# Optimization experiments

Hardware: AMD Instinct MI355X
Metric: run time of the kernel (lower is better)

Reference implementation:

```python
import jax, jax.numpy as jnp
import numpy as np


def setup_inputs() -> dict:
    key = jax.random.key(0)
    ks = jax.random.split(key, 8)
    B, C, D, H, W = 4, 128, 16, 16, 16
    Cqk = C // 8  # out_channels // 8 = 16
    return {
        "x": jax.random.normal(ks[0], (B, C, D, H, W), dtype=jnp.float32),
        "Wq": jax.random.normal(ks[1], (Cqk, C), dtype=jnp.float32) * 0.05,
        "bq": jax.random.normal(ks[2], (Cqk,), dtype=jnp.float32) * 0.05,
        "Wk": jax.random.normal(ks[3], (Cqk, C), dtype=jnp.float32) * 0.05,
        "bk": jax.random.normal(ks[4], (Cqk,), dtype=jnp.float32) * 0.05,
        "Wv": jax.random.normal(ks[5], (C, C), dtype=jnp.float32) * 0.05,
        "bv": jax.random.normal(ks[6], (C,), dtype=jnp.float32) * 0.05,
        "gamma": jax.random.normal(ks[7], (1,), dtype=jnp.float32),
    }


def reference(x, Wq, bq, Wk, bk, Wv, bv, gamma):
    B, C, D, H, W = x.shape
    xf = x.reshape(B, C, D * H * W)  # b c n
    # 1x1x1 Conv3d == channel-wise GEMM
    q = jnp.einsum('oc,bcn->bon', Wq, xf) + bq[None, :, None]  # [B, Cqk, N]
    k = jnp.einsum('oc,bcn->bon', Wk, xf) + bk[None, :, None]  # [B, Cqk, N]
    v = jnp.einsum('oc,bcn->bon', Wv, xf) + bv[None, :, None]  # [B, C,   N]
    # attention[b, n, m] = sum_c q[b,c,n] * k[b,c,m]  (NO 1/sqrt(d) scaling, faithful)
    attn = jax.nn.softmax(jnp.einsum('bcn,bcm->bnm', q, k), axis=-1)  # [B, N, N]
    out = jnp.einsum('bcm,bnm->bcn', v, attn)  # [B, C, N]
    out = out.reshape(B, C, D, H, W)
    return gamma * out + x
```

## Files before the change

### kernel.cpp

```cpp
#include <hip/hip_runtime.h>


typedef __attribute__((ext_vector_type(8))) short short8;
typedef __attribute__((ext_vector_type(4))) float f32x4;

#define NTOK 4096
#define CDIM 128
#define L2E 1.44269504088896340736f

__device__ __forceinline__ unsigned short f2bf(float f) {
  unsigned int u = __float_as_uint(f);
  return (unsigned short)((u + 0x7fffu + ((u >> 16) & 1u)) >> 16);
}

__global__ __launch_bounds__(256) void sa3d_proj(
    const float* __restrict__ x,
    const float* __restrict__ Wq, const float* __restrict__ bq,
    const float* __restrict__ Wk, const float* __restrict__ bk,
    const float* __restrict__ Wv, const float* __restrict__ bv,
    unsigned short* __restrict__ qb, unsigned short* __restrict__ kb,
    unsigned short* __restrict__ vb)
{
  __shared__ unsigned short Wl[160 * 136];
  __shared__ unsigned short xT[64 * 136];
  const int tid = threadIdx.x;
  const int b = (blockIdx.x & 7) >> 1;
  const int nt = ((blockIdx.x >> 3) << 1) | (blockIdx.x & 1);
  const int n0 = nt << 6;

  for (int i = 0; i < 80; ++i) {
    int idx = i * 256 + tid;
    int o = idx >> 7, c = idx & 127;
    float wv;
    if (o < 16)      wv = Wq[o * 128 + c] * L2E;
    else if (o < 32) wv = Wk[(o - 16) * 128 + c];
    else             wv = Wv[(o - 32) * 128 + c];
    Wl[o * 136 + c] = f2bf(wv);
  }
  {
    int nn = tid & 63, cg = tid >> 6;
    const float* xp = x + (size_t)b * CDIM * NTOK + n0 + nn;
    for (int cp = 0; cp < 16; ++cp) {
      int c = cg * 32 + cp * 2;
      float v0 = xp[(size_t)c * NTOK];
      float v1 = xp[(size_t)(c + 1) * NTOK];
      *(unsigned int*)&xT[nn * 136 + c] =
          (unsigned int)f2bf(v0) | ((unsigned int)f2bf(v1) << 16);
    }
  }
  __syncthreads();

  const int w = tid >> 6, lane = tid & 63;
  const int l15 = lane & 15, g = lane >> 4;

  short8 bfr[4];
#pragma unroll
  for (int ks = 0; ks < 4; ++ks)
    bfr[ks] = *(const short8*)&xT[(w * 16 + l15) * 136 + ks * 32 + g * 8];

  const int n = n0 + w * 16 + l15;
#pragma unroll
  for (int ot = 0; ot < 10; ++ot) {
    f32x4 acc = {};
#pragma unroll
    for (int ks = 0; ks < 4; ++ks) {
      short8 af = *(const short8*)&Wl[(ot * 16 + l15) * 136 + ks * 32 + g * 8];
      acc = __builtin_amdgcn_mfma_f32_16x16x32_bf16(af, bfr[ks], acc, 0, 0, 0);
    }
    int ob = ot * 16 + 4 * g;
    if (ot == 0) {
      unsigned int p0 = (unsigned int)f2bf(acc[0] + bq[ob] * L2E) |
                        ((unsigned int)f2bf(acc[1] + bq[ob + 1] * L2E) << 16);
      unsigned int p1 = (unsigned int)f2bf(acc[2] + bq[ob + 2] * L2E) |
                        ((unsigned int)f2bf(acc[3] + bq[ob + 3] * L2E) << 16);
      unsigned int* d = (unsigned int*)&qb[((size_t)b * NTOK + n) * 16 + ob];
      d[0] = p0; d[1] = p1;
    } else if (ot == 1) {
      int o2 = ob - 16;
      unsigned int p0 = (unsigned int)f2bf(acc[0] + bk[o2]) |
                        ((unsigned int)f2bf(acc[1] + bk[o2 + 1]) << 16);
      unsigned int p1 = (unsigned int)f2bf(acc[2] + bk[o2 + 2]) |
                        ((unsigned int)f2bf(acc[3] + bk[o2 + 3]) << 16);
      unsigned int* d = (unsigned int*)&kb[((size_t)b * NTOK + n) * 16 + o2];
      d[0] = p0; d[1] = p1;
    } else {
#pragma unroll
      for (int r = 0; r < 4; ++r) {
        int o = ob + r - 32;
        size_t eidx = (size_t)(n >> 6) * 8192 +
                      (size_t)((o >> 4) * 2 + ((n >> 5) & 1)) * 512 +
                      (size_t)((n >> 3) & 3) * 128 + (o & 15) * 8 + (n & 7);
        vb[(size_t)b * (CDIM * NTOK) + eidx] = f2bf(acc[r] + bv[o]);
      }
    }
  }
}

__global__ __launch_bounds__(512, 2) void sa3d_attn(
    const unsigned short* __restrict__ qb, const unsigned short* __restrict__ kb,
    const unsigned short* __restrict__ vb,
    const float* __restrict__ x, const float* __restrict__ gamma,
    float* __restrict__ out)
{
  __shared__ __align__(16) unsigned char smem[37888];

  const int tid = threadIdx.x;
  const int w = tid >> 6, lane = tid & 63;
  const int l15 = lane & 15, g = lane >> 4;
  const int kg = w >> 1, cg = w & 1;
  const int b = (blockIdx.x & 7) >> 1;
  const int qt = ((blockIdx.x >> 3) << 1) | (blockIdx.x & 1);
  const int q0 = qt << 5;

  unsigned short* PLk = (unsigned short*)smem + kg * 4608;
  float* LDp = (float*)(smem + 36864);

  const unsigned short* qbase = qb + (size_t)b * NTOK * 16;
  const unsigned short* kbase = kb + (size_t)b * NTOK * 16;
  const unsigned short* vbase = vb + (size_t)b * CDIM * NTOK;

  short8 aq[2] = {short8{}, short8{}};
#pragma unroll
  for (int qh = 0; qh < 2; ++qh)
    if (g < 2)
      aq[qh] = *(const short8*)&qbase[(size_t)(q0 + qh * 16 + l15) * 16 + g * 8];

  f32x4 acc[8];
#pragma unroll
  for (int i = 0; i < 8; ++i) acc[i] = (f32x4){};
  float Lp[2][4] = {{0.f, 0.f, 0.f, 0.f}, {0.f, 0.f, 0.f, 0.f}};

  const int kv0 = kg << 10;
  const int kcolb = cg * 32 + l15;
  const int voff = cg * 4096 + g * 128 + l15 * 8;
  const unsigned short* vtile = vbase + (size_t)kg * 16 * 8192;

  short8 kf[2];

#define LOADK(TT)                                                             \
  {                                                                           \
    _Pragma("unroll") for (int j = 0; j < 2; ++j) {                           \
      kf[j] = short8{};                                                       \
      if (g < 2)                                                              \
        kf[j] = *(const short8*)&kbase[                                       \
            (size_t)(kv0 + ((TT) << 6) + kcolb + j * 16) * 16 + g * 8];       \
    }                                                                         \
  }

#define SA_PRODUCE(TN)                                                        \
  {                                                                           \
    const int pbn = ((TN) & 1) * 2304;                                        \
    _Pragma("unroll") for (int j = 0; j < 2; ++j) {                           \
      _Pragma("unroll") for (int qh = 0; qh < 2; ++qh) {                      \
        f32x4 z = {};                                                         \
        f32x4 s = __builtin_amdgcn_mfma_f32_16x16x32_bf16(aq[qh], kf[j],      \
                                                          z, 0, 0, 0);        \
        float e0 = __builtin_exp2f(s[0]);                                     \
        float e1 = __builtin_exp2f(s[1]);                                     \
        float e2 = __builtin_exp2f(s[2]);                                     \
        float e3 = __builtin_exp2f(s[3]);                                     \
        Lp[qh][0] += e0; Lp[qh][1] += e1;                                     \
        Lp[qh][2] += e2; Lp[qh][3] += e3;                                     \
        unsigned int pk0, pk1;                                                \
        asm("v_cvt_pk_bf16_f32 %0, %1, %2" : "=v"(pk0) : "v"(e0), "v"(e1));   \
        asm("v_cvt_pk_bf16_f32 %0, %1, %2" : "=v"(pk1) : "v"(e2), "v"(e3));   \
        const int rb = pbn + (qh * 16 + 4 * g) * 72 + kcolb + j * 16;         \
        PLk[rb]       = (unsigned short)pk0;                                  \
        PLk[rb + 72]  = (unsigned short)(pk0 >> 16);                          \
        PLk[rb + 144] = (unsigned short)pk1;                                  \
        PLk[rb + 216] = (unsigned short)(pk1 >> 16);                          \
      }                                                                       \
    }                                                                         \
  }

#define SA_ITER(T, PROD, PREF)                                                \
  {                                                                           \
    const int pbo = ((T) & 1) * 2304;                                         \
    short8 pa0[2];                                                            \
    _Pragma("unroll") for (int ch = 0; ch < 2; ++ch)                          \
      pa0[ch] = *(const short8*)&PLk[pbo + l15 * 72 + ch * 32 + g * 8];       \
    short8 vf[8];                                                             \
    {                                                                         \
      const unsigned short* vt = vtile + (size_t)(T) * 8192;                  \
      _Pragma("unroll") for (int f = 0; f < 8; ++f)                           \
        vf[f] = *(const short8*)&vt[f * 512 + voff];                          \
    }                                                                         \
    if (PROD) SA_PRODUCE((T) + 1);                                            \
    if (PREF) LOADK((T) + 2);                                                 \
    __builtin_amdgcn_s_setprio(1);                                            \
    _Pragma("unroll") for (int ctl = 0; ctl < 4; ++ctl)                       \
      _Pragma("unroll") for (int ch = 0; ch < 2; ++ch)                        \
        acc[ctl] = __builtin_amdgcn_mfma_f32_16x16x32_bf16(                   \
            pa0[ch], vf[ctl * 2 + ch], acc[ctl], 0, 0, 0);                    \
    __builtin_amdgcn_s_setprio(0);                                            \
    short8 pa1[2];                                                            \
    _Pragma("unroll") for (int ch = 0; ch < 2; ++ch)                          \
      pa1[ch] = *(const short8*)&PLk[pbo + (16 + l15) * 72 + ch * 32 + g * 8];\
    __builtin_amdgcn_s_setprio(1);                                            \
    _Pragma("unroll") for (int ctl = 0; ctl < 4; ++ctl)                       \
      _Pragma("unroll") for (int ch = 0; ch < 2; ++ch)                        \
        acc[4 + ctl] = __builtin_amdgcn_mfma_f32_16x16x32_bf16(               \
            pa1[ch], vf[ctl * 2 + ch], acc[4 + ctl], 0, 0, 0);                \
    __builtin_amdgcn_s_setprio(0);                                            \
    __syncthreads();                                                          \
  }

  LOADK(0);
  SA_PRODUCE(0);
  LOADK(1);
  __syncthreads();

  for (int tt = 0; tt < 7; ++tt) {
    SA_ITER(2 * tt, 1, 1);
    SA_ITER(2 * tt + 1, 1, 1);
  }
  SA_ITER(14, 1, 0);
  SA_ITER(15, 0, 0);
#undef SA_PRODUCE
#undef SA_ITER
#undef LOADK

#pragma unroll
  for (int qh = 0; qh < 2; ++qh)
#pragma unroll
    for (int r = 0; r < 4; ++r) {
      float v = Lp[qh][r];
      v += __shfl_xor(v, 1);
      v += __shfl_xor(v, 2);
      v += __shfl_xor(v, 4);
      v += __shfl_xor(v, 8);
      Lp[qh][r] = v;
    }
  if (l15 == 0) {
#pragma unroll
    for (int qh = 0; qh < 2; ++qh)
#pragma unroll
      for (int r = 0; r < 4; ++r)
        LDp[w * 32 + qh * 16 + 4 * g + r] = Lp[qh][r];
  }
  __syncthreads();

  const int rowb = lane * 128;
  const int sw = (l15 & 7) << 4;

#define ACC_STORE(i)                                                        \
  {                                                                         \
    char* base = (char*)smem + (i) * 8192 + rowb;                           \
    _Pragma("unroll") for (int j = 0; j < 8; ++j)                           \
        *(f32x4*)(base + ((j * 16) ^ sw)) = acc[j];                         \
  }
#define ACC_ADD(i)                                                          \
  {                                                                         \
    char* base = (char*)smem + (i) * 8192 + rowb;                           \
    _Pragma("unroll") for (int j = 0; j < 8; ++j)                           \
        acc[j] += *(const f32x4*)(base + ((j * 16) ^ sw));                  \
  }

  if (w >= 4) ACC_STORE(w - 4);
  __syncthreads();
  if (w < 4) ACC_ADD(w);
  __syncthreads();
  if (w == 2 || w == 3) ACC_STORE(w - 2);
  __syncthreads();

  if (w < 2) {
    ACC_ADD(w);
    float Lf[2][4] = {{0.f, 0.f, 0.f, 0.f}, {0.f, 0.f, 0.f, 0.f}};
#pragma unroll
    for (int w8 = 0; w8 < 8; ++w8)
#pragma unroll
      for (int qh = 0; qh < 2; ++qh)
#pragma unroll
        for (int r = 0; r < 4; ++r)
          Lf[qh][r] += LDp[w8 * 32 + qh * 16 + 4 * g + r];
    const float ga = gamma[0];
    float inv[2][4];
#pragma unroll
    for (int qh = 0; qh < 2; ++qh)
#pragma unroll
      for (int r = 0; r < 4; ++r) inv[qh][r] = 1.0f / Lf[qh][r];

    const float* xb = x + (size_t)b * CDIM * NTOK;
    float* ob = out + (size_t)b * CDIM * NTOK;
#pragma unroll
    for (int qh = 0; qh < 2; ++qh)
#pragma unroll
      for (int ctl = 0; ctl < 4; ++ctl) {
        int c = w * 64 + ctl * 16 + l15;
        size_t idx = (size_t)c * NTOK + q0 + qh * 16 + 4 * g;
        f32x4 xv = *(const f32x4*)&xb[idx];
        f32x4 o;
#pragma unroll
        for (int r = 0; r < 4; ++r)
          o[r] = ga * acc[qh * 4 + ctl][r] * inv[qh][r] + xv[r];
        *(f32x4*)&ob[idx] = o;
      }
  }
}

extern "C" void kernel_launch(void* const* d_in, const int* in_sizes, int n_in,
                              void* d_out, int out_size, void* d_ws, size_t ws_size,
                              hipStream_t stream) {
  const float* x     = (const float*)d_in[0];
  const float* Wq    = (const float*)d_in[1];
  const float* bq    = (const float*)d_in[2];
  const float* Wk    = (const float*)d_in[3];
  const float* bk    = (const float*)d_in[4];
  const float* Wv    = (const float*)d_in[5];
  const float* bv    = (const float*)d_in[6];
  const float* gamma = (const float*)d_in[7];

  unsigned short* qb = (unsigned short*)d_ws;
  unsigned short* kb = qb + (size_t)4 * NTOK * 16;
  unsigned short* vb = kb + (size_t)4 * NTOK * 16;
  float* outp = (float*)d_out;

  sa3d_proj<<<dim3(256), dim3(256), 0, stream>>>(x, Wq, bq, Wk, bk, Wv, bv,
                                                 qb, kb, vb);
  sa3d_attn<<<dim3(512), dim3(512), 0, stream>>>(qb, kb, vb, x, gamma, outp);
}
```

Before: 69.67 us.

## Keep softmax probabilities in registers via transposed QK MFMA and lane shuffles

Computes S^T with K as the MFMA A operand so each wave produces the full probability tile for its own key range. It then rearranges the packed bf16 values into the PV A-operand layout with cross-lane shuffles instead of staging them through LDS. This removes the LDS P buffers and the per-tile __syncthreads, and shrinks shared memory. In exchange each wave now computes the QK^T tile for all 64 keys of a tile (double the QK MFMAs and exps per wave) and adds shuffle traffic and serial dependency between QK and PV within a wave.

```diff
diff --git a/kernel.cpp b/kernel.cpp
--- a/kernel.cpp
+++ b/kernel.cpp
@@ -3,6 +3,7 @@
 
 typedef __attribute__((ext_vector_type(8))) short short8;
 typedef __attribute__((ext_vector_type(4))) float f32x4;
+typedef __attribute__((ext_vector_type(4))) unsigned int u32x4;
 
 #define NTOK 4096
 #define CDIM 128
@@ -102,7 +103,7 @@
     const float* __restrict__ x, const float* __restrict__ gamma,
     float* __restrict__ out)
 {
-  __shared__ __align__(16) unsigned char smem[37888];
+  __shared__ __align__(16) unsigned char smem[33792];
 
   const int tid = threadIdx.x;
   const int w = tid >> 6, lane = tid & 63;
@@ -112,8 +113,7 @@
   const int qt = ((blockIdx.x >> 3) << 1) | (blockIdx.x & 1);
   const int q0 = qt << 5;
 
-  unsigned short* PLk = (unsigned short*)smem + kg * 4608;
-  float* LDp = (float*)(smem + 36864);
+  float* LDp = (float*)(smem + 32768);
 
   const unsigned short* qbase = qb + (size_t)b * NTOK * 16;
   const unsigned short* kbase = kb + (size_t)b * NTOK * 16;
@@ -128,109 +128,103 @@
   f32x4 acc[8];
 #pragma unroll
   for (int i = 0; i < 8; ++i) acc[i] = (f32x4){};
-  float Lp[2][4] = {{0.f, 0.f, 0.f, 0.f}, {0.f, 0.f, 0.f, 0.f}};
+  float Lq[2] = {0.f, 0.f};
 
   const int kv0 = kg << 10;
-  const int kcolb = cg * 32 + l15;
   const int voff = cg * 4096 + g * 128 + l15 * 8;
   const unsigned short* vtile = vbase + (size_t)kg * 16 * 8192;
 
-  short8 kf[2];
+  const bool hi32 = lane >= 32;
+  const int srcb = l15 + ((g & 1) << 5);
+
+  short8 kf[4];
 
 #define LOADK(TT)                                                             \
   {                                                                           \
-    _Pragma("unroll") for (int j = 0; j < 2; ++j) {                           \
+    _Pragma("unroll") for (int j = 0; j < 4; ++j) {                           \
       kf[j] = short8{};                                                       \
       if (g < 2)                                                              \
         kf[j] = *(const short8*)&kbase[                                       \
-            (size_t)(kv0 + ((TT) << 6) + kcolb + j * 16) * 16 + g * 8];       \
+            (size_t)(kv0 + ((TT) << 6) + j * 16 + l15) * 16 + g * 8];         \
     }                                                                         \
   }
 
-#define SA_PRODUCE(TN)                                                        \
+#define QK_HALF(HC, PA)                                                       \
   {                                                                           \
-    const int pbn = ((TN) & 1) * 2304;                                        \
-    _Pragma("unroll") for (int j = 0; j < 2; ++j) {                           \
+    unsigned int cpk[2][2][2];                           \
+    _Pragma("unroll") for (int kt2 = 0; kt2 < 2; ++kt2) {                     \
       _Pragma("unroll") for (int qh = 0; qh < 2; ++qh) {                      \
         f32x4 z = {};                                                         \
-        f32x4 s = __builtin_amdgcn_mfma_f32_16x16x32_bf16(aq[qh], kf[j],      \
-                                                          z, 0, 0, 0);        \
+        f32x4 s = __builtin_amdgcn_mfma_f32_16x16x32_bf16(                    \
+            kf[(HC) * 2 + kt2], aq[qh], z, 0, 0, 0);                          \
         float e0 = __builtin_exp2f(s[0]);                                     \
         float e1 = __builtin_exp2f(s[1]);                                     \
         float e2 = __builtin_exp2f(s[2]);                                     \
         float e3 = __builtin_exp2f(s[3]);                                     \
-        Lp[qh][0] += e0; Lp[qh][1] += e1;                                     \
-        Lp[qh][2] += e2; Lp[qh][3] += e3;                                     \
-        unsigned int pk0, pk1;                                                \
-        asm("v_cvt_pk_bf16_f32 %0, %1, %2" : "=v"(pk0) : "v"(e0), "v"(e1));   \
-        asm("v_cvt_pk_bf16_f32 %0, %1, %2" : "=v"(pk1) : "v"(e2), "v"(e3));   \
-        const int rb = pbn + (qh * 16 + 4 * g) * 72 + kcolb + j * 16;         \
-        PLk[rb]       = (unsigned short)pk0;                                  \
-        PLk[rb + 72]  = (unsigned short)(pk0 >> 16);                          \
-        PLk[rb + 144] = (unsigned short)pk1;                                  \
-        PLk[rb + 216] = (unsigned short)(pk1 >> 16);                          \
+        Lq[qh] += (e0 + e1) + (e2 + e3);                                      \
+        asm("v_cvt_pk_bf16_f32 %0, %1, %2"                                    \
+            : "=v"(cpk[qh][kt2][0]) : "v"(e0), "v"(e1));                      \
+        asm("v_cvt_pk_bf16_f32 %0, %1, %2"                                    \
+            : "=v"(cpk[qh][kt2][1]) : "v"(e2), "v"(e3));                      \
       }                                                                       \
     }                                                                         \
-  }
-
-#define SA_ITER(T, PROD, PREF)                                                \
+    _Pragma("unroll") for (int qh = 0; qh < 2; ++qh) {                        \
+      unsigned int selA = hi32 ? cpk[qh][1][0] : cpk[qh][0][0];               \
+      unsigned int selB = hi32 ? cpk[qh][1][1] : cpk[qh][0][1];               \
+      unsigned int w0 = (unsigned int)__shfl((int)selA, srcb);                \
+      unsigned int w1 = (unsigned int)__shfl((int)selB, srcb);                \
+      unsigned int w2 = (unsigned int)__shfl((int)selA, srcb + 16);           \
+      unsigned int w3 = (unsigned int)__shfl((int)selB, srcb + 16);           \
+      u32x4 pw = {w0, w1, w2, w3};                                            \
+      PA[qh] = *(short8*)&pw;                                                 \
+    }                                                                         \
+  }
+
+#define SA_TILE(T, PREF)                                                      \
   {                                                                           \
-    const int pbo = ((T) & 1) * 2304;                                         \
-    short8 pa0[2];                                                            \
-    _Pragma("unroll") for (int ch = 0; ch < 2; ++ch)                          \
-      pa0[ch] = *(const short8*)&PLk[pbo + l15 * 72 + ch * 32 + g * 8];       \
     short8 vf[8];                                                             \
     {                                                                         \
       const unsigned short* vt = vtile + (size_t)(T) * 8192;                  \
       _Pragma("unroll") for (int f = 0; f < 8; ++f)                           \
         vf[f] = *(const short8*)&vt[f * 512 + voff];                          \
     }                                                                         \
-    if (PROD) SA_PRODUCE((T) + 1);                                            \
-    if (PREF) LOADK((T) + 2);                                                 \
+    short8 pa[2];                                                             \
+    QK_HALF(0, pa);                                                           \
     __builtin_amdgcn_s_setprio(1);                                            \
-    _Pragma("unroll") for (int ctl = 0; ctl < 4; ++ctl)                       \
-      _Pragma("unroll") for (int ch = 0; ch < 2; ++ch)                        \
-        acc[ctl] = __builtin_amdgcn_mfma_f32_16x16x32_bf16(                   \
-            pa0[ch], vf[ctl * 2 + ch], acc[ctl], 0, 0, 0);                    \
+    _Pragma("unroll") for (int qh = 0; qh < 2; ++qh)                          \
+      _Pragma("unroll") for (int ctl = 0; ctl < 4; ++ctl)                     \
+        acc[qh * 4 + ctl] = __builtin_amdgcn_mfma_f32_16x16x32_bf16(          \
+            pa[qh], vf[ctl * 2 + 0], acc[qh * 4 + ctl], 0, 0, 0);             \
     __builtin_amdgcn_s_setprio(0);                                            \
-    short8 pa1[2];                                                            \
-    _Pragma("unroll") for (int ch = 0; ch < 2; ++ch)                          \
-      pa1[ch] = *(const short8*)&PLk[pbo + (16 + l15) * 72 + ch * 32 + g * 8];\
+    QK_HALF(1, pa);                                                           \
+    if (PREF) LOADK((T) + 1);                                                 \
     __builtin_amdgcn_s_setprio(1);                                            \
-    _Pragma("unroll") for (int ctl = 0; ctl < 4; ++ctl)                       \
-      _Pragma("unroll") for (int ch = 0; ch < 2; ++ch)                        \
-        acc[4 + ctl] = __builtin_amdgcn_mfma_f32_16x16x32_bf16(               \
-            pa1[ch], vf[ctl * 2 + ch], acc[4 + ctl], 0, 0, 0);                \
+    _Pragma("unroll") for (int qh = 0; qh < 2; ++qh)                          \
+      _Pragma("unroll") for (int ctl = 0; ctl < 4; ++ctl)                     \
+        acc[qh * 4 + ctl] = __builtin_amdgcn_mfma_f32_16x16x32_bf16(          \
+            pa[qh], vf[ctl * 2 + 1], acc[qh * 4 + ctl], 0, 0, 0);             \
     __builtin_amdgcn_s_setprio(0);                                            \
-    __syncthreads();                                                          \
   }
 
   LOADK(0);
-  SA_PRODUCE(0);
-  LOADK(1);
-  __syncthreads();
-
-  for (int tt = 0; tt < 7; ++tt) {
-    SA_ITER(2 * tt, 1, 1);
-    SA_ITER(2 * tt + 1, 1, 1);
-  }
-  SA_ITER(14, 1, 0);
-  SA_ITER(15, 0, 0);
-#undef SA_PRODUCE
-#undef SA_ITER
+  SA_TILE(0, 1);  SA_TILE(1, 1);  SA_TILE(2, 1);  SA_TILE(3, 1);
+  SA_TILE(4, 1);  SA_TILE(5, 1);  SA_TILE(6, 1);  SA_TILE(7, 1);
+  SA_TILE(8, 1);  SA_TILE(9, 1);  SA_TILE(10, 1); SA_TILE(11, 1);
+  SA_TILE(12, 1); SA_TILE(13, 1); SA_TILE(14, 1); SA_TILE(15, 0);
+#undef SA_TILE
+#undef QK_HALF
 #undef LOADK
 
-#pragma unroll
-  for (int qh = 0; qh < 2; ++qh)
-#pragma unroll
-    for (int r = 0; r < 4; ++r) {
-      float v = Lp[qh][r];
-      v += __shfl_xor(v, 1);
-      v += __shfl_xor(v, 2);
-      v += __shfl_xor(v, 4);
-      v += __shfl_xor(v, 8);
-      Lp[qh][r] = v;
-    }
+  float Lp[2][4];
+#pragma unroll
+  for (int qh = 0; qh < 2; ++qh) {
+    float v = Lq[qh];
+    v += __shfl_xor(v, 16);
+    v += __shfl_xor(v, 32);
+#pragma unroll
+    for (int r = 0; r < 4; ++r)
+      Lp[qh][r] = __shfl(v, 4 * g + r);
+  }
   if (l15 == 0) {
 #pragma unroll
     for (int qh = 0; qh < 2; ++qh)
```

New measurement: 197.7 us. +183.7%, slower.
